# Kernel tuning notes

Hardware: AMD Instinct MI355X
Metric: run time of the kernel (lower is better)

## Reference

```python
import jax, jax.numpy as jnp
import numpy as np

B, S, D = 4, 512, 768
MAX_LEN = 10        # max_span_len
LEN_EMB = 25        # span_len_embedding_dim
NUM_LABELS = 9      # len(labels.entities)
N = S * MAX_LEN     # all spans per sentence


def setup_inputs() -> dict:
    key = jax.random.key(0)
    k1, k2, k3 = jax.random.split(key, 3)
    word_embeddings = jax.random.normal(k1, (B, S, D), dtype=jnp.float32)
    # enumerate all spans (start, len) with len in [1, MAX_LEN], clamped at sentence end
    starts = jnp.repeat(jnp.arange(S, dtype=jnp.int32), MAX_LEN)            # [N]
    lens = jnp.tile(jnp.arange(1, MAX_LEN + 1, dtype=jnp.int32), S)          # [N]
    lens = jnp.minimum(lens, S - starts)
    span_starts = jnp.broadcast_to(starts, (B, N))
    span_lens = jnp.broadcast_to(lens, (B, N))
    len_emb_table = jax.random.normal(k2, (MAX_LEN, LEN_EMB), dtype=jnp.float32) * 0.02
    W = jax.random.normal(k3, (D + LEN_EMB, NUM_LABELS), dtype=jnp.float32) * 0.02
    b = jnp.zeros((NUM_LABELS,), dtype=jnp.float32)
    return {"word_embeddings": word_embeddings, "span_starts": span_starts,
            "span_lens": span_lens, "len_emb_table": len_emb_table, "W": W, "b": b}


def reference(word_embeddings, span_starts, span_lens, len_emb_table, W, b):
    # gather span tokens: [B, N, L, D]
    offs = jnp.arange(MAX_LEN, dtype=span_starts.dtype)                      # [L]
    idx = span_starts[:, :, None] + offs[None, None, :]                      # [B,N,L]
    mask = offs[None, None, :] < span_lens[:, :, None]                       # [B,N,L]
    idx = jnp.where(mask, idx, 0)                                            # keep in-bounds
    gathered = word_embeddings[jnp.arange(word_embeddings.shape[0])[:, None, None], idx]
    # masked max pooling over span tokens (every span has len >= 1)
    neg = jnp.asarray(-jnp.inf, dtype=gathered.dtype)
    pooled = jnp.max(jnp.where(mask[..., None], gathered, neg), axis=2)      # [B,N,D]
    # span-length embedding, indexed by (end - start - 1)
    len_emb = len_emb_table[span_lens - 1]                                   # [B,N,LEN_EMB]
    feat = jnp.concatenate([pooled, len_emb], axis=-1)                       # [B,N,D+LEN_EMB]
    logits = jnp.einsum('bnf,fc->bnc', feat, W) + b                          # [B,N,NUM_LABELS]
    return logits
```

## Files before the change

kernel.cpp:

```cpp
#include <hip/hip_runtime.h>
#include <hip/hip_bf16.h>
#include <stdint.h>

constexpr int kB = 4, kS = 512, kD = 768, kMaxLen = 10, kLenEmb = 25, kC = 9;
constexpr int kN = kS * kMaxLen;

__global__ __launch_bounds__(256) void span_ner_kernel(
    const float* __restrict__ emb,
    const int* __restrict__ starts,
    const int* __restrict__ lens,
    const float* __restrict__ len_tab,
    const float* __restrict__ W,
    const float* __restrict__ bias,
    float* __restrict__ out)
{
  __shared__ float lenAdd[kMaxLen][kC];
  const int t = threadIdx.x;
  if (t < kMaxLen * kC) {
    const int L = t / kC, c = t % kC;
    float s = bias[c];
    #pragma unroll
    for (int e = 0; e < kLenEmb; ++e)
      s = fmaf(len_tab[L * kLenEmb + e], W[(kD + e) * kC + c], s);
    lenAdd[L][c] = s;
  }
  __syncthreads();

  const int lane = t & 63;
  const int wid  = blockIdx.x * 4 + (t >> 6);
  const int b    = wid >> 9;
  const int s0   = wid & 511;

  float w[108];
  {
    const float4* wp = (const float4*)(W + lane * 108);
    #pragma unroll
    for (int i = 0; i < 27; ++i) {
      float4 u = wp[i];
      w[4 * i + 0] = u.x;
      w[4 * i + 1] = u.y;
      w[4 * i + 2] = u.z;
      w[4 * i + 3] = u.w;
    }
  }

  float pool[12];
  #pragma unroll
  for (int k = 0; k < 12; ++k) pool[k] = -INFINITY;

  const int base_n = s0 * kMaxLen;
  const int start  = starts[base_n];
  const float* rowbase = emb + (size_t)(b * kS + start) * kD + lane * 12;

  int rl = 0;
  for (int j = 0; j < kMaxLen; ++j) {
    int ln = lens[base_n + j];
    ln = min(max(ln, 1), kMaxLen);
    while (rl < ln) {
      const float4* rp = (const float4*)(rowbase + (size_t)rl * kD);
      #pragma unroll
      for (int i = 0; i < 3; ++i) {
        float4 u = rp[i];
        pool[4 * i + 0] = fmaxf(pool[4 * i + 0], u.x);
        pool[4 * i + 1] = fmaxf(pool[4 * i + 1], u.y);
        pool[4 * i + 2] = fmaxf(pool[4 * i + 2], u.z);
        pool[4 * i + 3] = fmaxf(pool[4 * i + 3], u.w);
      }
      ++rl;
    }

    float acc[kC];
    #pragma unroll
    for (int c = 0; c < kC; ++c) acc[c] = 0.f;
    #pragma unroll
    for (int k = 0; k < 12; ++k)
      #pragma unroll
      for (int c = 0; c < kC; ++c)
        acc[c] = fmaf(pool[k], w[k * kC + c], acc[c]);

    #pragma unroll
    for (int off = 32; off > 0; off >>= 1)
      #pragma unroll
      for (int c = 0; c < kC; ++c)
        acc[c] += __shfl_xor(acc[c], off, 64);

    float v = acc[0];
    #pragma unroll
    for (int c = 1; c < kC; ++c) v = (lane == c) ? acc[c] : v;
    if (lane < kC) {
      v += lenAdd[ln - 1][lane];
      out[(size_t)(b * kN + base_n + j) * kC + lane] = v;
    }
  }
}

extern "C" void kernel_launch(void* const* d_in, const int* in_sizes, int n_in,
                              void* d_out, int out_size, void* d_ws, size_t ws_size,
                              hipStream_t stream) {
  const float* emb     = (const float*)d_in[0];
  const int*   starts  = (const int*)d_in[1];
  const int*   lens    = (const int*)d_in[2];
  const float* len_tab = (const float*)d_in[3];
  const float* W       = (const float*)d_in[4];
  const float* bias    = (const float*)d_in[5];
  float*       out     = (float*)d_out;

  dim3 grid(kB * kS / 4);
  span_ner_kernel<<<grid, dim3(256), 0, stream>>>(emb, starts, lens, len_tab, W,
                                                  bias, out);
}
```

Before: 86.30 us.

## Use folding butterfly reduction for 9 logits and software-pipeline span rows

Replaces the 54-shuffle wavefront reduction of nine per-class partial sums with a folding reduction in which lanes exchange halves of the class set, so about 15 shuffles are needed and each class ends up in a specific lane. Output lanes are remapped through a lane-to-class table. The span loop is also unrolled and software-pipelined: the next row is prefetched and the next span's dot product runs before the previous span's reduction, to overlap load latency with shuffle work. This raises register pressure alongside the 108-float weight array already held per lane.

```diff
diff --git a/kernel.cpp b/kernel.cpp
--- a/kernel.cpp
+++ b/kernel.cpp
@@ -1,9 +1,47 @@
 #include <hip/hip_runtime.h>
-#include <hip/hip_bf16.h>
 #include <stdint.h>
 
 constexpr int kB = 4, kS = 512, kD = 768, kMaxLen = 10, kLenEmb = 25, kC = 9;
 constexpr int kN = kS * kMaxLen;
+
+__device__ __forceinline__ float reduce9_fold(const float acc[kC], int lane) {
+  float s0 = acc[0] + __shfl_xor(acc[0], 1, 64);
+  float s1 = acc[1] + __shfl_xor(acc[1], 1, 64);
+  float s2 = acc[2] + __shfl_xor(acc[2], 1, 64);
+  float s3 = acc[3] + __shfl_xor(acc[3], 1, 64);
+  float s4 = acc[4] + __shfl_xor(acc[4], 1, 64);
+  float s5 = acc[5] + __shfl_xor(acc[5], 1, 64);
+  float s6 = acc[6] + __shfl_xor(acc[6], 1, 64);
+  float s7 = acc[7] + __shfl_xor(acc[7], 1, 64);
+  float s8 = acc[8] + __shfl_xor(acc[8], 1, 64);
+  const bool o1 = (lane & 1) != 0;
+  const bool o2 = (lane & 2) != 0;
+  const bool o4 = (lane & 4) != 0;
+  const bool o8 = (lane & 8) != 0;
+  float b0 = o1 ? s5 : s0;
+  float b1 = o1 ? s6 : s1;
+  float b2 = o1 ? s7 : s2;
+  float b3 = o1 ? s8 : s3;
+  float b4 = s4;
+  float u0 = b0 + __shfl_xor(b0, 2, 64);
+  float u1 = b1 + __shfl_xor(b1, 2, 64);
+  float u2 = b2 + __shfl_xor(b2, 2, 64);
+  float u3 = b3 + __shfl_xor(b3, 2, 64);
+  float u4 = b4 + __shfl_xor(b4, 2, 64);
+  float q0 = o2 ? u3 : u0;
+  float q1 = o2 ? u4 : u1;
+  float q2 = u2;
+  float v0 = q0 + __shfl_xor(q0, 4, 64);
+  float v1 = q1 + __shfl_xor(q1, 4, 64);
+  float v2 = q2 + __shfl_xor(q2, 4, 64);
+  float d0 = o4 ? v2 : v0;
+  float d1 = v1;
+  float w0 = d0 + __shfl_xor(d0, 8, 64);
+  float w1 = d1 + __shfl_xor(d1, 8, 64);
+  float e0 = o8 ? w1 : w0;
+  float f0 = e0 + __shfl_xor(e0, 16, 64);
+  return f0 + __shfl_xor(f0, 32, 64);
+}
 
 __global__ __launch_bounds__(256) void span_ner_kernel(
     const float* __restrict__ emb,
@@ -31,6 +69,20 @@
   const int b    = wid >> 9;
   const int s0   = wid & 511;
 
+  int myc = -1;
+  switch (lane) {
+    case 0:  myc = 0; break;
+    case 8:  myc = 1; break;
+    case 4:  myc = 2; break;
+    case 2:  myc = 3; break;
+    case 10: myc = 4; break;
+    case 1:  myc = 5; break;
+    case 9:  myc = 6; break;
+    case 5:  myc = 7; break;
+    case 3:  myc = 8; break;
+    default: break;
+  }
+
   float w[108];
   {
     const float4* wp = (const float4*)(W + lane * 108);
@@ -44,32 +96,49 @@
     }
   }
 
+  const int base_n = s0 * kMaxLen;
+
+  int lnv[kMaxLen];
+  #pragma unroll
+  for (int j = 0; j < kMaxLen; ++j) {
+    int ln = lens[base_n + j];
+    lnv[j] = min(max(ln, 1), kMaxLen);
+  }
+  const int start = starts[base_n];
+  const float* rowbase = emb + (size_t)(b * kS + start) * kD + lane * 12;
+
   float pool[12];
   #pragma unroll
   for (int k = 0; k < 12; ++k) pool[k] = -INFINITY;
-
-  const int base_n = s0 * kMaxLen;
-  const int start  = starts[base_n];
-  const float* rowbase = emb + (size_t)(b * kS + start) * kD + lane * 12;
-
-  int rl = 0;
-  for (int j = 0; j < kMaxLen; ++j) {
-    int ln = lens[base_n + j];
-    ln = min(max(ln, 1), kMaxLen);
-    while (rl < ln) {
-      const float4* rp = (const float4*)(rowbase + (size_t)rl * kD);
-      #pragma unroll
-      for (int i = 0; i < 3; ++i) {
-        float4 u = rp[i];
-        pool[4 * i + 0] = fmaxf(pool[4 * i + 0], u.x);
-        pool[4 * i + 1] = fmaxf(pool[4 * i + 1], u.y);
-        pool[4 * i + 2] = fmaxf(pool[4 * i + 2], u.z);
-        pool[4 * i + 3] = fmaxf(pool[4 * i + 3], u.w);
-      }
-      ++rl;
-    }
-
-    float acc[kC];
+  float rn[12];
+
+  auto loadfold = [&](int r) {
+    const float4* rp = (const float4*)(rowbase + (size_t)r * kD);
+    #pragma unroll
+    for (int i = 0; i < 3; ++i) {
+      float4 u = rp[i];
+      pool[4 * i + 0] = fmaxf(pool[4 * i + 0], u.x);
+      pool[4 * i + 1] = fmaxf(pool[4 * i + 1], u.y);
+      pool[4 * i + 2] = fmaxf(pool[4 * i + 2], u.z);
+      pool[4 * i + 3] = fmaxf(pool[4 * i + 3], u.w);
+    }
+  };
+  auto loadrn = [&](int r) {
+    const float4* rp = (const float4*)(rowbase + (size_t)r * kD);
+    #pragma unroll
+    for (int i = 0; i < 3; ++i) {
+      float4 u = rp[i];
+      rn[4 * i + 0] = u.x;
+      rn[4 * i + 1] = u.y;
+      rn[4 * i + 2] = u.z;
+      rn[4 * i + 3] = u.w;
+    }
+  };
+  auto foldrn = [&]() {
+    #pragma unroll
+    for (int k = 0; k < 12; ++k) pool[k] = fmaxf(pool[k], rn[k]);
+  };
+  auto dot9 = [&](float acc[kC]) {
     #pragma unroll
     for (int c = 0; c < kC; ++c) acc[c] = 0.f;
     #pragma unroll
@@ -77,19 +146,39 @@
       #pragma unroll
       for (int c = 0; c < kC; ++c)
         acc[c] = fmaf(pool[k], w[k * kC + c], acc[c]);
-
-    #pragma unroll
-    for (int off = 32; off > 0; off >>= 1)
-      #pragma unroll
-      for (int c = 0; c < kC; ++c)
-        acc[c] += __shfl_xor(acc[c], off, 64);
-
-    float v = acc[0];
-    #pragma unroll
-    for (int c = 1; c < kC; ++c) v = (lane == c) ? acc[c] : v;
-    if (lane < kC) {
-      v += lenAdd[ln - 1][lane];
-      out[(size_t)(b * kN + base_n + j) * kC + lane] = v;
+  };
+
+  int rl = 0;
+  while (rl < lnv[0]) { loadfold(rl); ++rl; }
+  bool pf = (rl < lnv[1]);
+  if (pf) loadrn(rl);
+
+  float accA[kC];
+  dot9(accA);
+
+  #pragma unroll
+  for (int j = 1; j < kMaxLen; ++j) {
+    if (pf) { foldrn(); ++rl; pf = false; }
+    while (rl < lnv[j]) { loadfold(rl); ++rl; }
+    if (j + 1 < kMaxLen) {
+      pf = (rl < lnv[j + 1]);
+      if (pf) loadrn(rl);
+    }
+    float accB[kC];
+    dot9(accB);
+    float g = reduce9_fold(accA, lane);
+    if (myc >= 0) {
+      out[(size_t)(b * kN + base_n + (j - 1)) * kC + myc] =
+          g + lenAdd[lnv[j - 1] - 1][myc];
+    }
+    #pragma unroll
+    for (int c = 0; c < kC; ++c) accA[c] = accB[c];
+  }
+  {
+    float g = reduce9_fold(accA, lane);
+    if (myc >= 0) {
+      out[(size_t)(b * kN + base_n + (kMaxLen - 1)) * kC + myc] =
+          g + lenAdd[lnv[kMaxLen - 1] - 1][myc];
     }
   }
 }
```

New measurement: 82.20 us. 1.05x faster.
